# Performance work log

Hardware: AMD Instinct MI355X
Metric: run time of the kernel (lower is better)

## Reference

```python
import jax, jax.numpy as jnp
import numpy as np

VOCAB, EMBED, SEQ, UNITS, BATCH = 10000, 100, 80, 64, 16384


def setup_inputs() -> dict:
    key = jax.random.key(0)
    ks = jax.random.split(key, 8)
    s = 0.05
    return {
        "tokens": jax.random.randint(ks[0], (BATCH, SEQ), 0, VOCAB, dtype=jnp.int32),
        "emb": jax.random.normal(ks[1], (VOCAB, EMBED), jnp.float32) * s,
        "Wx1": jax.random.normal(ks[2], (EMBED, UNITS), jnp.float32) * s,
        "Wh1": jax.random.normal(ks[3], (UNITS, UNITS), jnp.float32) * s,
        "b1": jnp.zeros((UNITS,), jnp.float32),
        "Wx2": jax.random.normal(ks[4], (UNITS, UNITS), jnp.float32) * s,
        "Wh2": jax.random.normal(ks[5], (UNITS, UNITS), jnp.float32) * s,
        "b2": jnp.zeros((UNITS,), jnp.float32),
        "Wd": jax.random.normal(ks[6], (UNITS, 1), jnp.float32) * s,
        "bd": jnp.zeros((1,), jnp.float32),
    }


def _simple_rnn(x, Wx, Wh, b):
    """SimpleRNN (eval mode): h_t = tanh(x_t @ Wx + h_{t-1} @ Wh + b).
    x: (B, T, E) -> all hidden states (B, T, U)."""
    # precompute input projection once (big GEMM), scan only does the small recurrent matmul
    xp = jnp.einsum("bte,eu->btu", x, Wx) + b  # (B, T, U)

    def step(h, xt):
        h = jnp.tanh(xt + h @ Wh)
        return h, h

    h0 = jnp.zeros((x.shape[0], Wh.shape[0]), x.dtype)
    _, hs = jax.lax.scan(step, h0, jnp.swapaxes(xp, 0, 1))  # (T, B, U)
    return jnp.swapaxes(hs, 0, 1)  # (B, T, U)


def reference(tokens, emb, Wx1, Wh1, b1, Wx2, Wh2, b2, Wd, bd):
    x = emb[tokens]                              # (B, T, E) embedding lookup
    h1 = _simple_rnn(x, Wx1, Wh1, b1)            # (B, T, U) return_sequences=True
    h2 = _simple_rnn(h1, Wx2, Wh2, b2)[:, -1]    # (B, U)    last state only
    return jax.nn.sigmoid(h2 @ Wd + bd)          # (B, 1)
```

## Files before the change

kernel.cpp:

```cpp
#include <hip/hip_runtime.h>
#include <hip/hip_bf16.h>


#define BATCH 16384
#define SEQ   80
#define EMBED 100
#define UNITS 64
#define ROWS  16
#define VOCAB 10000
#define EPAD  128

typedef __attribute__((ext_vector_type(8))) short bf16x8;
typedef __attribute__((ext_vector_type(4))) float f32x4;
typedef __attribute__((ext_vector_type(2))) float f32x2;
typedef __attribute__((ext_vector_type(4))) int   i32x4;
typedef __attribute__((ext_vector_type(2))) int   i32x2;

static __device__ __forceinline__ unsigned short bf16_rne(float f) {
    unsigned u = __builtin_bit_cast(unsigned, f);
    u += 0x7FFFu + ((u >> 16) & 1u);
    return (unsigned short)(u >> 16);
}

static __device__ __forceinline__ float bf16_to_f(short s) {
    unsigned u = ((unsigned)(unsigned short)s) << 16;
    return __builtin_bit_cast(float, u);
}

static __device__ __forceinline__ int pack_bf16(float a, float b) {
    unsigned ua = __builtin_bit_cast(unsigned, a) + 0x8000u;
    unsigned ub = __builtin_bit_cast(unsigned, b) + 0x8000u;
    return (int)__builtin_amdgcn_perm(ub, ua, 0x07060302u);
}

static __device__ __forceinline__ f32x2 tanh2(f32x2 x) {
    f32x2 u = x * x;
    f32x2 w = x * u;
    f32x2 p = u * 0.13333333f + (-0.33333333f);
    return w * p + x;
}

static __device__ __forceinline__ i32x2 tanh_pack4(f32x4 v) {
    f32x2 lo = tanh2((f32x2){v[0], v[1]});
    f32x2 hi = tanh2((f32x2){v[2], v[3]});
    i32x2 r;
    r[0] = pack_bf16(lo[0], lo[1]);
    r[1] = pack_bf16(hi[0], hi[1]);
    return r;
}

static __device__ __forceinline__ bf16x8 asb(i32x4 v) {
    return __builtin_bit_cast(bf16x8, v);
}

__global__ __launch_bounds__(256) void emb_prep(const float* __restrict__ emb,
                                                unsigned short* __restrict__ embb) {
    int i = blockIdx.x * 256 + threadIdx.x;
    if (i < VOCAB * EPAD) {
        int v = i >> 7, k = i & (EPAD - 1);
        float f = (k < EMBED) ? emb[v * EMBED + k] : 0.0f;
        embb[i] = bf16_rne(f);
    }
}

template <bool BF16EMB>
__global__ __launch_bounds__(64, 1)
void rnn_fused(const int* __restrict__ tokens,
               const float* __restrict__ emb,
               const unsigned short* __restrict__ embb,
               const float* __restrict__ Wx1,
               const float* __restrict__ Wh1,
               const float* __restrict__ b1,
               const float* __restrict__ Wx2,
               const float* __restrict__ Wh2,
               const float* __restrict__ b2,
               const float* __restrict__ Wd,
               const float* __restrict__ bd,
               float* __restrict__ out)
{
    __shared__ int tokL[ROWS][SEQ + 1];

    const int lane = threadIdx.x;
    const int c = lane & 15;
    const int q = lane >> 4;
    const int rowBase = blockIdx.x * ROWS;

    for (int i = lane; i < ROWS * SEQ; i += 64) {
        int r = i / SEQ, tt = i - r * SEQ;
        tokL[r][tt] = tokens[rowBase * SEQ + i];
    }
    __syncthreads();

    bf16x8 awx1[4][4];
#pragma unroll
    for (int kt = 0; kt < 4; ++kt)
#pragma unroll
        for (int mt = 0; mt < 4; ++mt) {
            bf16x8 v;
#pragma unroll
            for (int j = 0; j < 8; ++j) {
                int k = kt * 32 + q * 8 + j;
                v[j] = (k < EMBED) ? (short)bf16_rne(Wx1[k * UNITS + mt * 16 + c]) : (short)0;
            }
            awx1[kt][mt] = v;
        }
    bf16x8 awh1[2][4], awx2[2][4], awh2[2][4];
#pragma unroll
    for (int kt = 0; kt < 2; ++kt)
#pragma unroll
        for (int mt = 0; mt < 4; ++mt) {
            bf16x8 va, vb, vc;
#pragma unroll
            for (int j = 0; j < 8; ++j) {
                int u = kt * 32 + ((j >> 2) << 4) + q * 4 + (j & 3);
                va[j] = (short)bf16_rne(Wh1[u * UNITS + mt * 16 + c]);
                vb[j] = (short)bf16_rne(Wx2[u * UNITS + mt * 16 + c]);
                vc[j] = (short)bf16_rne(Wh2[u * UNITS + mt * 16 + c]);
            }
            awh1[kt][mt] = va; awx2[kt][mt] = vb; awh2[kt][mt] = vc;
        }
    f32x4 b1C[4], b2C[4];
#pragma unroll
    for (int mt = 0; mt < 4; ++mt)
#pragma unroll
        for (int r = 0; r < 4; ++r) {
            b1C[mt][r] = b1[mt * 16 + q * 4 + r];
            b2C[mt][r] = b2[mt * 16 + q * 4 + r];
        }

    i32x4 h1B[2] = {(i32x4){0,0,0,0}, (i32x4){0,0,0,0}};
    i32x4 h2B[2] = {(i32x4){0,0,0,0}, (i32x4){0,0,0,0}};

    i32x4 xB[4][4];
    auto gatherX = [&](int token, i32x4 (&xg)[4]) {
        if constexpr (BF16EMB) {
            const unsigned short* eb = embb + (size_t)token * EPAD + q * 8;
#pragma unroll
            for (int kt = 0; kt < 4; ++kt)
                xg[kt] = *reinterpret_cast<const i32x4*>(eb + kt * 32);
        } else {
            const float* eb = emb + (size_t)token * EMBED;
#pragma unroll
            for (int kt = 0; kt < 4; ++kt) {
                int k0 = kt * 32 + q * 8;
                f32x4 a = (k0 < EMBED)     ? *reinterpret_cast<const f32x4*>(eb + k0)
                                           : (f32x4){0.f, 0.f, 0.f, 0.f};
                f32x4 b = (k0 + 4 < EMBED) ? *reinterpret_cast<const f32x4*>(eb + k0 + 4)
                                           : (f32x4){0.f, 0.f, 0.f, 0.f};
                i32x4 v;
                v[0] = pack_bf16(a[0], a[1]);
                v[1] = pack_bf16(a[2], a[3]);
                v[2] = pack_bf16(b[0], b[1]);
                v[3] = pack_bf16(b[2], b[3]);
                xg[kt] = v;
            }
        }
    };

    f32x4 xc0[4], xc1[4];
    auto buildXC = [&](i32x4 (&xr)[4], f32x4 (&xcW)[4]) {
#pragma unroll
        for (int mt = 0; mt < 4; ++mt)
            xcW[mt] = __builtin_amdgcn_mfma_f32_16x16x32_bf16(awx1[0][mt], asb(xr[0]), b1C[mt], 0, 0, 0);
#pragma unroll
        for (int kt = 1; kt < 4; ++kt)
#pragma unroll
            for (int mt = 0; mt < 4; ++mt)
                xcW[mt] = __builtin_amdgcn_mfma_f32_16x16x32_bf16(awx1[kt][mt], asb(xr[kt]), xcW[mt], 0, 0, 0);
    };

    gatherX(tokL[c][0], xB[0]);
    gatherX(tokL[c][1], xB[1]);
    gatherX(tokL[c][2], xB[2]);
    buildXC(xB[0], xc0);

    auto iter = [&](int t, f32x4 (&xcR)[4], f32x4 (&xcW)[4], int rs, int ws,
                    bool pubH2, bool doG, bool doXC) {
        f32x4 a2[4];
#pragma unroll
        for (int mt = 0; mt < 4; ++mt)
            a2[mt] = __builtin_amdgcn_mfma_f32_16x16x32_bf16(awx2[0][mt], asb(h1B[0]), b2C[mt], 0, 0, 0);
#pragma unroll
        for (int mt = 0; mt < 4; ++mt)
            a2[mt] = __builtin_amdgcn_mfma_f32_16x16x32_bf16(awh2[0][mt], asb(h2B[0]), a2[mt], 0, 0, 0);
#pragma unroll
        for (int mt = 0; mt < 4; ++mt)
            a2[mt] = __builtin_amdgcn_mfma_f32_16x16x32_bf16(awx2[1][mt], asb(h1B[1]), a2[mt], 0, 0, 0);
#pragma unroll
        for (int mt = 0; mt < 4; ++mt)
            a2[mt] = __builtin_amdgcn_mfma_f32_16x16x32_bf16(awh2[1][mt], asb(h2B[1]), a2[mt], 0, 0, 0);

        f32x4 a1[4];
#pragma unroll
        for (int mt = 0; mt < 4; ++mt)
            a1[mt] = __builtin_amdgcn_mfma_f32_16x16x32_bf16(awh1[0][mt], asb(h1B[0]), xcR[mt], 0, 0, 0);
#pragma unroll
        for (int mt = 0; mt < 4; ++mt)
            a1[mt] = __builtin_amdgcn_mfma_f32_16x16x32_bf16(awh1[1][mt], asb(h1B[1]), a1[mt], 0, 0, 0);

        if (doG) gatherX(tokL[c][t + 3], xB[ws]);

        if (doXC) buildXC(xB[rs], xcW);

        i32x2 p0 = tanh_pack4(a1[0]), p1 = tanh_pack4(a1[1]);
        i32x2 p2 = tanh_pack4(a1[2]), p3 = tanh_pack4(a1[3]);
        if (pubH2) {
            i32x2 s0 = tanh_pack4(a2[0]), s1 = tanh_pack4(a2[1]);
            i32x2 s2 = tanh_pack4(a2[2]), s3 = tanh_pack4(a2[3]);
            h2B[0] = (i32x4){s0[0], s0[1], s1[0], s1[1]};
            h2B[1] = (i32x4){s2[0], s2[1], s3[0], s3[1]};
        }
        h1B[0] = (i32x4){p0[0], p0[1], p1[0], p1[1]};
        h1B[1] = (i32x4){p2[0], p2[1], p3[0], p3[1]};
    };

    iter(0, xc0, xc1, 1, 3, false, true, true);
    iter(1, xc1, xc0, 2, 0, true,  true, true);
    iter(2, xc0, xc1, 3, 1, true,  true, true);
    iter(3, xc1, xc0, 0, 2, true,  true, true);

#pragma unroll 1
    for (int tt = 4; tt <= 72; tt += 4) {
        iter(tt + 0, xc0, xc1, 1, 3, true, true, true);
        iter(tt + 1, xc1, xc0, 2, 0, true, true, true);
        iter(tt + 2, xc0, xc1, 3, 1, true, true, true);
        iter(tt + 3, xc1, xc0, 0, 2, true, true, true);
    }

    iter(76, xc0, xc1, 1, 3, true, true,  true);
    iter(77, xc1, xc0, 2, 0, true, false, true);
    iter(78, xc0, xc1, 3, 1, true, false, true);
    iter(79, xc1, xc0, 0, 2, true, false, false);

    f32x4 a2[4];
#pragma unroll
    for (int mt = 0; mt < 4; ++mt)
        a2[mt] = __builtin_amdgcn_mfma_f32_16x16x32_bf16(awx2[0][mt], asb(h1B[0]), b2C[mt], 0, 0, 0);
#pragma unroll
    for (int mt = 0; mt < 4; ++mt)
        a2[mt] = __builtin_amdgcn_mfma_f32_16x16x32_bf16(awh2[0][mt], asb(h2B[0]), a2[mt], 0, 0, 0);
#pragma unroll
    for (int mt = 0; mt < 4; ++mt)
        a2[mt] = __builtin_amdgcn_mfma_f32_16x16x32_bf16(awx2[1][mt], asb(h1B[1]), a2[mt], 0, 0, 0);
#pragma unroll
    for (int mt = 0; mt < 4; ++mt)
        a2[mt] = __builtin_amdgcn_mfma_f32_16x16x32_bf16(awh2[1][mt], asb(h2B[1]), a2[mt], 0, 0, 0);

    i32x2 s0 = tanh_pack4(a2[0]), s1 = tanh_pack4(a2[1]);
    i32x2 s2 = tanh_pack4(a2[2]), s3 = tanh_pack4(a2[3]);
    h2B[0] = (i32x4){s0[0], s0[1], s1[0], s1[1]};
    h2B[1] = (i32x4){s2[0], s2[1], s3[0], s3[1]};

    float p = 0.f;
#pragma unroll
    for (int kt = 0; kt < 2; ++kt) {
        bf16x8 hb = asb(h2B[kt]);
#pragma unroll
        for (int j = 0; j < 8; ++j) {
            int u = kt * 32 + ((j >> 2) << 4) + q * 4 + (j & 3);
            p += bf16_to_f(hb[j]) * Wd[u];
        }
    }
    p += __shfl_xor(p, 16);
    p += __shfl_xor(p, 32);
    if (q == 0) {
        float x = p + bd[0];
        out[rowBase + c] = __builtin_amdgcn_rcpf(1.0f + __expf(-x));
    }
}

extern "C" void kernel_launch(void* const* d_in, const int* in_sizes, int n_in,
                              void* d_out, int out_size, void* d_ws, size_t ws_size,
                              hipStream_t stream) {
    const int*   tokens = (const int*)  d_in[0];
    const float* emb    = (const float*)d_in[1];
    const float* Wx1    = (const float*)d_in[2];
    const float* Wh1    = (const float*)d_in[3];
    const float* b1     = (const float*)d_in[4];
    const float* Wx2    = (const float*)d_in[5];
    const float* Wh2    = (const float*)d_in[6];
    const float* b2     = (const float*)d_in[7];
    const float* Wd     = (const float*)d_in[8];
    const float* bd     = (const float*)d_in[9];
    float* out = (float*)d_out;

    dim3 grid(BATCH / ROWS);
    dim3 block(64);
    const size_t embb_bytes = (size_t)VOCAB * EPAD * sizeof(unsigned short);
    if (ws_size >= embb_bytes) {
        unsigned short* embb = (unsigned short*)d_ws;
        emb_prep<<<dim3((VOCAB * EPAD + 255) / 256), dim3(256), 0, stream>>>(emb, embb);
        rnn_fused<true><<<grid, block, 0, stream>>>(tokens, emb, embb, Wx1, Wh1, b1,
                                                    Wx2, Wh2, b2, Wd, bd, out);
    } else {
        rnn_fused<false><<<grid, block, 0, stream>>>(tokens, emb, nullptr, Wx1, Wh1, b1,
                                                     Wx2, Wh2, b2, Wd, bd, out);
    }
}
```

Measured before the change: 156.3 us.

## Precompute per-vocab input projection table instead of per-token MFMA projection

Since the layer-1 input projection depends only on the token, a prep kernel now computes emb@Wx1+b1 once for all 10000 vocab rows in fp32, and the RNN kernel gathers 64 floats per token instead of gathering embeddings and running 16 MFMAs per step. This removes the Wx1 register fragments and the per-step projection MFMAs from the recurrent loop, which lowers register pressure and work on the critical path. In exchange it adds a small prep GEMM over the vocabulary and a larger fp32 gather table, and it shortens the prefetch distance to two steps.

New measurement: 170.9 us. 1.09x slower.

```diff
diff --git a/kernel.cpp b/kernel.cpp
--- a/kernel.cpp
+++ b/kernel.cpp
@@ -8,7 +8,6 @@
 #define UNITS 64
 #define ROWS  16
 #define VOCAB 10000
-#define EPAD  128
 
 typedef __attribute__((ext_vector_type(8))) short bf16x8;
 typedef __attribute__((ext_vector_type(4))) float f32x4;
@@ -53,21 +52,31 @@
     return __builtin_bit_cast(bf16x8, v);
 }
 
-__global__ __launch_bounds__(256) void emb_prep(const float* __restrict__ emb,
-                                                unsigned short* __restrict__ embb) {
-    int i = blockIdx.x * 256 + threadIdx.x;
-    if (i < VOCAB * EPAD) {
-        int v = i >> 7, k = i & (EPAD - 1);
-        float f = (k < EMBED) ? emb[v * EMBED + k] : 0.0f;
-        embb[i] = bf16_rne(f);
-    }
-}
-
-template <bool BF16EMB>
+__global__ __launch_bounds__(256) void xp_prep(const float* __restrict__ emb,
+                                               const float* __restrict__ Wx1,
+                                               const float* __restrict__ b1,
+                                               float* __restrict__ xp) {
+    const int v = blockIdx.x * 4 + (threadIdx.x >> 6);
+    const int u = threadIdx.x & 63;
+    const float* er = emb + (size_t)v * EMBED;
+    const float* wc = Wx1 + u;
+    float acc = b1[u];
+#pragma unroll 5
+    for (int k4 = 0; k4 < EMBED / 4; ++k4) {
+        f32x4 e = *reinterpret_cast<const f32x4*>(er + k4 * 4);
+        acc += e[0] * wc[(k4 * 4 + 0) * UNITS];
+        acc += e[1] * wc[(k4 * 4 + 1) * UNITS];
+        acc += e[2] * wc[(k4 * 4 + 2) * UNITS];
+        acc += e[3] * wc[(k4 * 4 + 3) * UNITS];
+    }
+    xp[(size_t)v * UNITS + u] = acc;
+}
+
+template <bool XP>
 __global__ __launch_bounds__(64, 1)
 void rnn_fused(const int* __restrict__ tokens,
                const float* __restrict__ emb,
-               const unsigned short* __restrict__ embb,
+               const float* __restrict__ xpT,
                const float* __restrict__ Wx1,
                const float* __restrict__ Wh1,
                const float* __restrict__ b1,
@@ -91,19 +100,6 @@
     }
     __syncthreads();
 
-    bf16x8 awx1[4][4];
-#pragma unroll
-    for (int kt = 0; kt < 4; ++kt)
-#pragma unroll
-        for (int mt = 0; mt < 4; ++mt) {
-            bf16x8 v;
-#pragma unroll
-            for (int j = 0; j < 8; ++j) {
-                int k = kt * 32 + q * 8 + j;
-                v[j] = (k < EMBED) ? (short)bf16_rne(Wx1[k * UNITS + mt * 16 + c]) : (short)0;
-            }
-            awx1[kt][mt] = v;
-        }
     bf16x8 awh1[2][4], awx2[2][4], awh2[2][4];
 #pragma unroll
     for (int kt = 0; kt < 2; ++kt)
@@ -119,63 +115,85 @@
             }
             awh1[kt][mt] = va; awx2[kt][mt] = vb; awh2[kt][mt] = vc;
         }
-    f32x4 b1C[4], b2C[4];
-#pragma unroll
-    for (int mt = 0; mt < 4; ++mt)
-#pragma unroll
-        for (int r = 0; r < 4; ++r) {
-            b1C[mt][r] = b1[mt * 16 + q * 4 + r];
+    f32x4 b2C[4];
+#pragma unroll
+    for (int mt = 0; mt < 4; ++mt)
+#pragma unroll
+        for (int r = 0; r < 4; ++r)
             b2C[mt][r] = b2[mt * 16 + q * 4 + r];
-        }
+
+    bf16x8 awx1[4][4];
+    f32x4 b1C[4];
+    if constexpr (!XP) {
+#pragma unroll
+        for (int kt = 0; kt < 4; ++kt)
+#pragma unroll
+            for (int mt = 0; mt < 4; ++mt) {
+                bf16x8 v;
+#pragma unroll
+                for (int j = 0; j < 8; ++j) {
+                    int k = kt * 32 + q * 8 + j;
+                    v[j] = (k < EMBED) ? (short)bf16_rne(Wx1[k * UNITS + mt * 16 + c])
+                                       : (short)0;
+                }
+                awx1[kt][mt] = v;
+            }
+#pragma unroll
+        for (int mt = 0; mt < 4; ++mt)
+#pragma unroll
+            for (int r = 0; r < 4; ++r)
+                b1C[mt][r] = b1[mt * 16 + q * 4 + r];
+    }
 
     i32x4 h1B[2] = {(i32x4){0,0,0,0}, (i32x4){0,0,0,0}};
     i32x4 h2B[2] = {(i32x4){0,0,0,0}, (i32x4){0,0,0,0}};
 
-    i32x4 xB[4][4];
-    auto gatherX = [&](int token, i32x4 (&xg)[4]) {
-        if constexpr (BF16EMB) {
-            const unsigned short* eb = embb + (size_t)token * EPAD + q * 8;
-#pragma unroll
-            for (int kt = 0; kt < 4; ++kt)
-                xg[kt] = *reinterpret_cast<const i32x4*>(eb + kt * 32);
-        } else {
-            const float* eb = emb + (size_t)token * EMBED;
-#pragma unroll
-            for (int kt = 0; kt < 4; ++kt) {
-                int k0 = kt * 32 + q * 8;
-                f32x4 a = (k0 < EMBED)     ? *reinterpret_cast<const f32x4*>(eb + k0)
-                                           : (f32x4){0.f, 0.f, 0.f, 0.f};
-                f32x4 b = (k0 + 4 < EMBED) ? *reinterpret_cast<const f32x4*>(eb + k0 + 4)
-                                           : (f32x4){0.f, 0.f, 0.f, 0.f};
-                i32x4 v;
-                v[0] = pack_bf16(a[0], a[1]);
-                v[1] = pack_bf16(a[2], a[3]);
-                v[2] = pack_bf16(b[0], b[1]);
-                v[3] = pack_bf16(b[2], b[3]);
-                xg[kt] = v;
-            }
-        }
+    f32x4 xpC[2][4];
+    auto gatherXP = [&](int t, f32x4 (&dst)[4]) {
+        int token = tokL[c][t];
+        const float* p = xpT + (size_t)token * UNITS + q * 4;
+        dst[0] = *reinterpret_cast<const f32x4*>(p);
+        dst[1] = *reinterpret_cast<const f32x4*>(p + 16);
+        dst[2] = *reinterpret_cast<const f32x4*>(p + 32);
+        dst[3] = *reinterpret_cast<const f32x4*>(p + 48);
     };
-
-    f32x4 xc0[4], xc1[4];
-    auto buildXC = [&](i32x4 (&xr)[4], f32x4 (&xcW)[4]) {
-#pragma unroll
-        for (int mt = 0; mt < 4; ++mt)
-            xcW[mt] = __builtin_amdgcn_mfma_f32_16x16x32_bf16(awx1[0][mt], asb(xr[0]), b1C[mt], 0, 0, 0);
+    auto buildXC = [&](int t, f32x4 (&dst)[4]) {
+        int token = tokL[c][t];
+        const float* eb = emb + (size_t)token * EMBED;
+        i32x4 xg[4];
+#pragma unroll
+        for (int kt = 0; kt < 4; ++kt) {
+            int k0 = kt * 32 + q * 8;
+            f32x4 a = (k0 < EMBED)     ? *reinterpret_cast<const f32x4*>(eb + k0)
+                                       : (f32x4){0.f, 0.f, 0.f, 0.f};
+            f32x4 b = (k0 + 4 < EMBED) ? *reinterpret_cast<const f32x4*>(eb + k0 + 4)
+                                       : (f32x4){0.f, 0.f, 0.f, 0.f};
+            i32x4 v;
+            v[0] = pack_bf16(a[0], a[1]);
+            v[1] = pack_bf16(a[2], a[3]);
+            v[2] = pack_bf16(b[0], b[1]);
+            v[3] = pack_bf16(b[2], b[3]);
+            xg[kt] = v;
+        }
+#pragma unroll
+        for (int mt = 0; mt < 4; ++mt)
+            dst[mt] = __builtin_amdgcn_mfma_f32_16x16x32_bf16(awx1[0][mt], asb(xg[0]), b1C[mt], 0, 0, 0);
 #pragma unroll
         for (int kt = 1; kt < 4; ++kt)
 #pragma unroll
             for (int mt = 0; mt < 4; ++mt)
-                xcW[mt] = __builtin_amdgcn_mfma_f32_16x16x32_bf16(awx1[kt][mt], asb(xr[kt]), xcW[mt], 0, 0, 0);
+                dst[mt] = __builtin_amdgcn_mfma_f32_16x16x32_bf16(awx1[kt][mt], asb(xg[kt]), dst[mt], 0, 0, 0);
     };
 
-    gatherX(tokL[c][0], xB[0]);
-    gatherX(tokL[c][1], xB[1]);
-    gatherX(tokL[c][2], xB[2]);
-    buildXC(xB[0], xc0);
-
-    auto iter = [&](int t, f32x4 (&xcR)[4], f32x4 (&xcW)[4], int rs, int ws,
-                    bool pubH2, bool doG, bool doXC) {
+    if constexpr (XP) {
+        gatherXP(0, xpC[0]);
+        gatherXP(1, xpC[1]);
+    } else {
+        buildXC(0, xpC[0]);
+        buildXC(1, xpC[1]);
+    }
+
+    auto iter = [&](int t, f32x4 (&xcR)[4], bool pubH2, bool doPre) {
         f32x4 a2[4];
 #pragma unroll
         for (int mt = 0; mt < 4; ++mt)
@@ -198,9 +216,10 @@
         for (int mt = 0; mt < 4; ++mt)
             a1[mt] = __builtin_amdgcn_mfma_f32_16x16x32_bf16(awh1[1][mt], asb(h1B[1]), a1[mt], 0, 0, 0);
 
-        if (doG) gatherX(tokL[c][t + 3], xB[ws]);
-
-        if (doXC) buildXC(xB[rs], xcW);
+        if (doPre) {
+            if constexpr (XP) gatherXP(t + 2, xcR);
+            else              buildXC(t + 2, xcR);
+        }
 
         i32x2 p0 = tanh_pack4(a1[0]), p1 = tanh_pack4(a1[1]);
         i32x2 p2 = tanh_pack4(a1[2]), p3 = tanh_pack4(a1[3]);
@@ -214,23 +233,15 @@
         h1B[1] = (i32x4){p2[0], p2[1], p3[0], p3[1]};
     };
 
-    iter(0, xc0, xc1, 1, 3, false, true, true);
-    iter(1, xc1, xc0, 2, 0, true,  true, true);
-    iter(2, xc0, xc1, 3, 1, true,  true, true);
-    iter(3, xc1, xc0, 0, 2, true,  true, true);
-
+    iter(0, xpC[0], false, true);
+    iter(1, xpC[1], true,  true);
 #pragma unroll 1
-    for (int tt = 4; tt <= 72; tt += 4) {
-        iter(tt + 0, xc0, xc1, 1, 3, true, true, true);
-        iter(tt + 1, xc1, xc0, 2, 0, true, true, true);
-        iter(tt + 2, xc0, xc1, 3, 1, true, true, true);
-        iter(tt + 3, xc1, xc0, 0, 2, true, true, true);
-    }
-
-    iter(76, xc0, xc1, 1, 3, true, true,  true);
-    iter(77, xc1, xc0, 2, 0, true, false, true);
-    iter(78, xc0, xc1, 3, 1, true, false, true);
-    iter(79, xc1, xc0, 0, 2, true, false, false);
+    for (int tt = 2; tt <= 76; tt += 2) {
+        iter(tt,     xpC[0], true, true);
+        iter(tt + 1, xpC[1], true, true);
+    }
+    iter(78, xpC[0], true, false);
+    iter(79, xpC[1], true, false);
 
     f32x4 a2[4];
 #pragma unroll
@@ -286,11 +297,11 @@
 
     dim3 grid(BATCH / ROWS);
     dim3 block(64);
-    const size_t embb_bytes = (size_t)VOCAB * EPAD * sizeof(unsigned short);
-    if (ws_size >= embb_bytes) {
-        unsigned short* embb = (unsigned short*)d_ws;
-        emb_prep<<<dim3((VOCAB * EPAD + 255) / 256), dim3(256), 0, stream>>>(emb, embb);
-        rnn_fused<true><<<grid, block, 0, stream>>>(tokens, emb, embb, Wx1, Wh1, b1,
+    const size_t xp_bytes = (size_t)VOCAB * UNITS * sizeof(float);
+    if (ws_size >= xp_bytes) {
+        float* xp = (float*)d_ws;
+        xp_prep<<<dim3(VOCAB / 4), dim3(256), 0, stream>>>(emb, Wx1, b1, xp);
+        rnn_fused<true><<<grid, block, 0, stream>>>(tokens, emb, xp, Wx1, Wh1, b1,
                                                     Wx2, Wh2, b2, Wd, bd, out);
     } else {
         rnn_fused<false><<<grid, block, 0, stream>>>(tokens, emb, nullptr, Wx1, Wh1, b1,
```
